# Optimization experiments

Hardware: AMD Instinct MI355X
Metric: run time of the kernel (lower is better)

## Reference

```python
import jax, jax.numpy as jnp
import numpy as np

B, S, I, H, O, L = 64, 512, 256, 512, 256, 2


def setup_inputs() -> dict:
    key = jax.random.key(0)
    ks = jax.random.split(key, 8)
    s = 0.02
    return {
        "x": jax.random.normal(ks[0], (B, S, I), dtype=jnp.float32),
        "input_W": jax.random.normal(ks[1], (H, I), dtype=jnp.float32) * s,
        "input_b": jnp.zeros((H,), dtype=jnp.float32),
        "i2h_W": jax.random.normal(ks[2], (L, H, H), dtype=jnp.float32) * s,
        "h2h_W": jax.random.normal(ks[3], (L, H, H), dtype=jnp.float32) * s,
        "h2h_b": jnp.zeros((L, H), dtype=jnp.float32),
        "out_W": jax.random.normal(ks[4], (O, H), dtype=jnp.float32) * s,
        "out_b": jnp.zeros((O,), dtype=jnp.float32),
    }


def reference(x, input_W, input_b, i2h_W, h2h_W, h2h_b, out_W, out_b):
    # input projection applied to the whole sequence at once, as in the source
    xe = jnp.einsum("bsi,hi->bsh", x, input_W) + input_b  # [B,S,H]

    def step(h, x_t):  # h: [L,B,H], x_t: [B,H]
        cur = x_t
        new_h = []
        for l in range(L):
            cur = jnp.tanh(cur @ i2h_W[l].T + h[l] @ h2h_W[l].T + h2h_b[l])
            new_h.append(cur)
        return jnp.stack(new_h), None

    h0 = jnp.zeros((L, B, H), dtype=x.dtype)
    hT, _ = jax.lax.scan(step, h0, jnp.swapaxes(xe, 0, 1))  # scan over S
    output = hT[-1] @ out_W.T + out_b  # [B,O]
    return output, hT
```

## Files before the change

### kernel.cpp

```cpp
#include <hip/hip_runtime.h>

typedef __attribute__((ext_vector_type(8))) short bf16x8;
typedef __attribute__((ext_vector_type(4))) float f32x4;

#define NWG 128

__device__ __forceinline__ unsigned short f2bf(float f) {
  union { float f; unsigned u; } v; v.f = f;
  unsigned r = v.u + 0x7FFFu + ((v.u >> 16) & 1u);
  return (unsigned short)(r >> 16);
}

__device__ __forceinline__ float bf2f(unsigned short u) {
  union { unsigned u; float f; } v; v.u = (unsigned)u << 16;
  return v.f;
}

__device__ __forceinline__ float fast_tanh(float x) {
  float ax = fminf(fabsf(x), 15.f);
  float e = __expf(2.f * ax);
  float t = (e - 1.f) / (e + 1.f);
  return copysignf(t, x);
}

#define LDH(d, b, O) \
  asm volatile("global_load_dwordx4 %0, %1, off offset:" #O " sc1" : "=v"(d) : "v"(b))
#define LDH16(A, B)            \
  LDH(A[0], B, 0);   LDH(A[1], B, 64);  LDH(A[2], B, 128); LDH(A[3], B, 192);  \
  LDH(A[4], B, 256); LDH(A[5], B, 320); LDH(A[6], B, 384); LDH(A[7], B, 448);  \
  LDH(A[8], B, 512); LDH(A[9], B, 576); LDH(A[10], B, 640); LDH(A[11], B, 704); \
  LDH(A[12], B, 768); LDH(A[13], B, 832); LDH(A[14], B, 896); LDH(A[15], B, 960)

__device__ __forceinline__ void wait_flags(const unsigned* p, unsigned tgt) {
  while (true) {
    unsigned v;
    asm volatile("global_load_dword %0, %1, off sc1\n\t"
                 "s_waitcnt vmcnt(0)"
                 : "=v"(v) : "v"(p) : "memory");
    if (__all((int)(v >= tgt))) break;
  }
}

__global__ void prep_kernel(const float* __restrict__ i2h,
                            const float* __restrict__ h2h,
                            unsigned short* __restrict__ WiB,
                            unsigned short* __restrict__ WhB,
                            unsigned short* __restrict__ h0,
                            unsigned short* __restrict__ h1,
                            unsigned* __restrict__ bar,
                            unsigned* __restrict__ flags) {
  int i = blockIdx.x * 256 + threadIdx.x;
  WiB[i] = f2bf(i2h[i]);
  WhB[i] = f2bf(h2h[i]);
  if (i < 65536) { h0[i] = 0; h1[i] = 0; }
  if (i < 64) bar[i] = 0;
  if (i < 4096) flags[i] = 0;
}

__global__ __launch_bounds__(256) void wc_kernel(const float* __restrict__ inW,
                                                 const float* __restrict__ inb,
                                                 const float* __restrict__ i2h,
                                                 const float* __restrict__ hb,
                                                 unsigned short* __restrict__ WcB,
                                                 float* __restrict__ bc) {
  const int n = blockIdx.x, i = threadIdx.x;
  const float* wrow = i2h + (size_t)n * 512;
  float acc = 0.f;
  for (int k = 0; k < 512; ++k) acc += wrow[k] * inW[k * 256 + i];
  WcB[n * 256 + i] = f2bf(acc);
  if (i == 0) {
    float a2 = 0.f;
    for (int k = 0; k < 512; ++k) a2 += wrow[k] * inb[k];
    bc[n] = a2 + hb[n];
  }
}

__global__ __launch_bounds__(256) void proj_kernel(const float* __restrict__ x,
                                                   const unsigned short* __restrict__ WcB,
                                                   const float* __restrict__ bc,
                                                   unsigned short* __restrict__ U) {
  const int tid = threadIdx.x;
  const int ln = tid & 63, wv = tid >> 6;
  const int wid = blockIdx.x * 4 + wv;
  const int mt = wid >> 5, nt = wid & 31;
  const int mrow = ln & 15, quad = ln >> 4, koff = quad * 8;
  const float* arow = x + (size_t)(mt * 16 + mrow) * 256 + koff;
  const unsigned short* brow = WcB + (size_t)(nt * 16 + mrow) * 256 + koff;
  f32x4 acc = {0.f, 0.f, 0.f, 0.f};
#pragma unroll
  for (int kk = 0; kk < 8; ++kk) {
    const int ko = kk * 32;
    bf16x8 af;
#pragma unroll
    for (int j = 0; j < 8; ++j) af[j] = (short)f2bf(arow[ko + j]);
    bf16x8 bf = *(const bf16x8*)(brow + ko);
    acc = __builtin_amdgcn_mfma_f32_16x16x32_bf16(af, bf, acc, 0, 0, 0);
  }
  const int n = nt * 16 + mrow;
  const float bias = bc[n];
  const int m0 = mt * 16 + quad * 4;
#pragma unroll
  for (int r = 0; r < 4; ++r) {
    const int m = m0 + r;
    const int b = m >> 9, s = m & 511;
    U[((size_t)(s * 64 + b) << 9) + n] = f2bf(acc[r] + bias);
  }
}

__device__ __forceinline__ void heavy_barrier(unsigned* bar) {
  __builtin_amdgcn_s_waitcnt(0);
  __syncthreads();
  if (threadIdx.x == 0) {
    __threadfence();
    unsigned prev = __hip_atomic_fetch_add(bar, 1u, __ATOMIC_RELAXED, __HIP_MEMORY_SCOPE_AGENT);
    if (prev == NWG - 1) {
      __hip_atomic_store(bar + 32, 1u, __ATOMIC_RELAXED, __HIP_MEMORY_SCOPE_AGENT);
    } else {
      while (__hip_atomic_load(bar + 32, __ATOMIC_RELAXED, __HIP_MEMORY_SCOPE_AGENT) < 1u)
        __builtin_amdgcn_s_sleep(1);
    }
    __threadfence();
  }
  __syncthreads();
}

__device__ __forceinline__ void store_h_coh(unsigned* dbase, int rowbase, int colp,
                                            bool evenl,
                                            float v0, float v1, float v2, float v3) {
  unsigned lo = (unsigned)f2bf(v0) | ((unsigned)f2bf(v1) << 16);
  unsigned hi = (unsigned)f2bf(v2) | ((unsigned)f2bf(v3) << 16);
  unsigned send = evenl ? hi : lo;
  unsigned recv = __shfl_xor(send, 1, 64);
  unsigned w0, w1; int rb;
  if (evenl) {
    w0 = (lo & 0xffffu) | (recv << 16);
    w1 = (lo >> 16) | (recv & 0xffff0000u);
    rb = rowbase;
  } else {
    w0 = (recv & 0xffffu) | (hi << 16);
    w1 = (recv >> 16) | (hi & 0xffff0000u);
    rb = rowbase + 2;
  }
  unsigned* p = dbase + rb * 256 + colp;
  __hip_atomic_store(p, w0, __ATOMIC_RELAXED, __HIP_MEMORY_SCOPE_AGENT);
  __hip_atomic_store(p + 256, w1, __ATOMIC_RELAXED, __HIP_MEMORY_SCOPE_AGENT);
}

__global__ __launch_bounds__(64, 1) void scan_kernel(const unsigned short* __restrict__ U,
                                                     const unsigned short* __restrict__ WiB,
                                                     const unsigned short* __restrict__ WhB,
                                                     const float* __restrict__ hb,
                                                     const float* __restrict__ outW,
                                                     const float* __restrict__ outb,
                                                     unsigned short* __restrict__ h0,
                                                     unsigned short* __restrict__ h1,
                                                     float* __restrict__ out,
                                                     unsigned* __restrict__ bar,
                                                     unsigned* __restrict__ flags) {
  const int ln = threadIdx.x;
  const int wid = blockIdx.x;
  const int rt = wid & 3;
  const int ct = wid >> 2;
  const int mrow = ln & 15, quad = ln >> 4, koff = quad * 8;
  const int bA = rt * 16 + mrow;
  const int n = ct * 16 + mrow;
  const bool evenl = (ln & 1) == 0;
  const int colp = n >> 1;
  const int rowbase = rt * 16 + quad * 4;

  bf16x8 wf0[16], wf1[16], wf2[16];
  {
    const unsigned short* w0 = WhB + (size_t)n * 512 + koff;
    const unsigned short* w1 = WiB + (size_t)262144 + (size_t)n * 512 + koff;
    const unsigned short* w2 = WhB + (size_t)262144 + (size_t)n * 512 + koff;
#pragma unroll
    for (int kk = 0; kk < 16; ++kk) {
      wf0[kk] = *(const bf16x8*)(w0 + kk * 32);
      wf1[kk] = *(const bf16x8*)(w1 + kk * 32);
      wf2[kk] = *(const bf16x8*)(w2 + kk * 32);
    }
  }
  const float bias1 = hb[512 + n];
  const unsigned short* h0b = h0 + (size_t)bA * 512 + koff;
  const unsigned short* h1b = h1 + (size_t)bA * 512 + koff;
  const unsigned short* UB = U + ((size_t)rowbase << 9) + n;
  unsigned* myflag = flags + ((rt * 32 + ct) << 5);
  const unsigned* pollp = flags + ((rt * 32 + (ln & 31)) << 5);

  unsigned short up0 = UB[0], up1 = UB[512], up2 = UB[1024], up3 = UB[1536];

  for (int s = 0; s <= 512; ++s) {
    const int pd = s & 1, ps = pd ^ 1;
    const bool D0 = (s < 512), D1 = (s > 0);
    if (s) wait_flags(pollp, (unsigned)s);

    const unsigned short* aH0 = h0b + (ps << 15);
    const unsigned short* aH1 = h1b + (pd << 15);
    bf16x8 h0f[16], h1f[16];
    LDH16(h0f, aH0);
    LDH16(h1f, aH1);

    asm volatile("s_waitcnt vmcnt(16)" ::: "memory");
#pragma unroll
    for (int kk = 0; kk < 16; ++kk) asm volatile("" : "+v"(h0f[kk]));

    f32x4 z = {0.f, 0.f, 0.f, 0.f};
    f32x4 acc0 = z, a1a = z, a1b = z;
#pragma unroll
    for (int kk = 0; kk < 16; ++kk) {
      if (D0) acc0 = __builtin_amdgcn_mfma_f32_16x16x32_bf16(h0f[kk], wf0[kk], acc0, 0, 0, 0);
      if (D1) a1a = __builtin_amdgcn_mfma_f32_16x16x32_bf16(h0f[kk], wf1[kk], a1a, 0, 0, 0);
    }

    if (D0) {
      float v0 = fast_tanh(acc0[0] + bf2f(up0));
      float v1 = fast_tanh(acc0[1] + bf2f(up1));
      float v2 = fast_tanh(acc0[2] + bf2f(up2));
      float v3 = fast_tanh(acc0[3] + bf2f(up3));
      store_h_coh((unsigned*)h0 + (pd << 14), rowbase, colp, evenl, v0, v1, v2, v3);
      if (s == 511) {
        float* o = out + 16384 + rowbase * 512 + n;
        o[0] = v0; o[512] = v1; o[1024] = v2; o[1536] = v3;
      }
    }

    if (D1) {
      asm volatile("s_waitcnt vmcnt(0)" ::: "memory");
#pragma unroll
      for (int kk = 0; kk < 16; ++kk) asm volatile("" : "+v"(h1f[kk]));
#pragma unroll
      for (int kk = 0; kk < 16; ++kk)
        a1b = __builtin_amdgcn_mfma_f32_16x16x32_bf16(h1f[kk], wf2[kk], a1b, 0, 0, 0);
      float v0 = fast_tanh(a1a[0] + a1b[0] + bias1);
      float v1 = fast_tanh(a1a[1] + a1b[1] + bias1);
      float v2 = fast_tanh(a1a[2] + a1b[2] + bias1);
      float v3 = fast_tanh(a1a[3] + a1b[3] + bias1);
      store_h_coh((unsigned*)h1 + (ps << 14), rowbase, colp, evenl, v0, v1, v2, v3);
      if (s == 512) {
        float* o = out + 16384 + 32768 + rowbase * 512 + n;
        o[0] = v0; o[512] = v1; o[1024] = v2; o[1536] = v3;
      }
    }

    asm volatile("s_waitcnt vmcnt(0)" ::: "memory");
    if (ln == 0) {
      unsigned fv = (unsigned)(s + 1);
      asm volatile("global_store_dword %0, %1, off sc1" :: "v"(myflag), "v"(fv) : "memory");
    }

    if (s <= 510) {
      const unsigned short* un = UB + ((size_t)(s + 1) << 15);
      up0 = un[0]; up1 = un[512]; up2 = un[1024]; up3 = un[1536];
    }
  }

  heavy_barrier(bar);

  const int g = blockIdx.x * 64 + ln;
  const float* hT1 = out + 16384 + 32768;
#pragma unroll
  for (int e = 0; e < 2; ++e) {
    const int idx = g + e * 8192;
    const int b = idx >> 8, o = idx & 255;
    const float* hr = hT1 + (b << 9);
    const float* wr = outW + (o << 9);
    float s0 = 0.f, s1 = 0.f;
    for (int k = 0; k < 512; k += 8) {
      float4 h4 = *(const float4*)(hr + k);
      float4 w4 = *(const float4*)(wr + k);
      s0 += h4.x * w4.x + h4.y * w4.y + h4.z * w4.z + h4.w * w4.w;
      float4 h5 = *(const float4*)(hr + k + 4);
      float4 w5 = *(const float4*)(wr + k + 4);
      s1 += h5.x * w5.x + h5.y * w5.y + h5.z * w5.z + h5.w * w5.w;
    }
    out[idx] = s0 + s1 + outb[o];
  }
}

extern "C" void kernel_launch(void* const* d_in, const int* in_sizes, int n_in,
                              void* d_out, int out_size, void* d_ws, size_t ws_size,
                              hipStream_t stream) {
  const float* x = (const float*)d_in[0];
  const float* inW = (const float*)d_in[1];
  const float* inb = (const float*)d_in[2];
  const float* i2h = (const float*)d_in[3];
  const float* h2h = (const float*)d_in[4];
  const float* hbias = (const float*)d_in[5];
  const float* outW = (const float*)d_in[6];
  const float* outb = (const float*)d_in[7];
  float* out = (float*)d_out;

  char* w = (char*)d_ws;
  unsigned short* WiB = (unsigned short*)w;
  unsigned short* WhB = (unsigned short*)(w + (1u << 20));
  unsigned short* WcB = (unsigned short*)(w + (2u << 20));
  float* bc = (float*)(w + (2u << 20) + (256u << 10));
  unsigned short* h0 = (unsigned short*)(w + (2u << 20) + (260u << 10));
  unsigned short* h1 = (unsigned short*)(w + (2u << 20) + (388u << 10));
  unsigned* bar = (unsigned*)(w + (2u << 20) + (516u << 10));
  unsigned* flags = (unsigned*)(w + (2u << 20) + (520u << 10));
  unsigned short* U = (unsigned short*)(w + (2u << 20) + (576u << 10));

  prep_kernel<<<2048, 256, 0, stream>>>(i2h, h2h, WiB, WhB, h0, h1, bar, flags);
  wc_kernel<<<512, 256, 0, stream>>>(inW, inb, i2h, hbias, WcB, bc);
  proj_kernel<<<16384, 256, 0, stream>>>(x, WcB, bc, U);
  scan_kernel<<<NWG, 64, 0, stream>>>(U, WiB, WhB, hbias, outW, outb, h0, h1, out, bar, flags);
}
```

Baseline: 2.109 ms.

## Split scan over 256 workgroups with XCC-local fast coherence path

Doubles the scan grid to 256 single-wave workgroups, each now owning 8 batch rows instead of 16, so per-step work is spread over more CUs. At startup it reads the XCC id of each workgroup and checks whether all groups sharing a batch tile sit on the same XCC. It then tests flag and data visibility with plain loads after buffer_inv. If that test passes, the recurrence loop uses non-sc1 stores and loads, which avoids device-scope coherence traffic. Otherwise it falls back to the sc1 path. This adds a startup handshake, bounded spin budgets that could silently break out early, and half the MFMA rows go to waste.

```diff
diff --git a/kernel.cpp b/kernel.cpp
--- a/kernel.cpp
+++ b/kernel.cpp
@@ -3,7 +3,9 @@
 typedef __attribute__((ext_vector_type(8))) short bf16x8;
 typedef __attribute__((ext_vector_type(4))) float f32x4;
 
-#define NWG 128
+#define NWG 256
+
+template <bool B> struct BoolC { static constexpr bool value = B; };
 
 __device__ __forceinline__ unsigned short f2bf(float f) {
   union { float f; unsigned u; } v; v.f = f;
@@ -23,21 +25,67 @@
   return copysignf(t, x);
 }
 
-#define LDH(d, b, O) \
+#define LDH_F(d, b, O) \
+  asm volatile("global_load_dwordx4 %0, %1, off offset:" #O : "=v"(d) : "v"(b))
+#define LDH_S(d, b, O) \
   asm volatile("global_load_dwordx4 %0, %1, off offset:" #O " sc1" : "=v"(d) : "v"(b))
-#define LDH16(A, B)            \
-  LDH(A[0], B, 0);   LDH(A[1], B, 64);  LDH(A[2], B, 128); LDH(A[3], B, 192);  \
-  LDH(A[4], B, 256); LDH(A[5], B, 320); LDH(A[6], B, 384); LDH(A[7], B, 448);  \
-  LDH(A[8], B, 512); LDH(A[9], B, 576); LDH(A[10], B, 640); LDH(A[11], B, 704); \
-  LDH(A[12], B, 768); LDH(A[13], B, 832); LDH(A[14], B, 896); LDH(A[15], B, 960)
-
-__device__ __forceinline__ void wait_flags(const unsigned* p, unsigned tgt) {
+#define LDH16_F(A, B)            \
+  LDH_F(A[0], B, 0);   LDH_F(A[1], B, 64);  LDH_F(A[2], B, 128); LDH_F(A[3], B, 192);  \
+  LDH_F(A[4], B, 256); LDH_F(A[5], B, 320); LDH_F(A[6], B, 384); LDH_F(A[7], B, 448);  \
+  LDH_F(A[8], B, 512); LDH_F(A[9], B, 576); LDH_F(A[10], B, 640); LDH_F(A[11], B, 704); \
+  LDH_F(A[12], B, 768); LDH_F(A[13], B, 832); LDH_F(A[14], B, 896); LDH_F(A[15], B, 960)
+#define LDH16_S(A, B)            \
+  LDH_S(A[0], B, 0);   LDH_S(A[1], B, 64);  LDH_S(A[2], B, 128); LDH_S(A[3], B, 192);  \
+  LDH_S(A[4], B, 256); LDH_S(A[5], B, 320); LDH_S(A[6], B, 384); LDH_S(A[7], B, 448);  \
+  LDH_S(A[8], B, 512); LDH_S(A[9], B, 576); LDH_S(A[10], B, 640); LDH_S(A[11], B, 704); \
+  LDH_S(A[12], B, 768); LDH_S(A[13], B, 832); LDH_S(A[14], B, 896); LDH_S(A[15], B, 960)
+
+template <bool FAST>
+__device__ __forceinline__ void poll_flags(const unsigned* p, unsigned tgt, int& budget) {
   while (true) {
     unsigned v;
-    asm volatile("global_load_dword %0, %1, off sc1\n\t"
-                 "s_waitcnt vmcnt(0)"
-                 : "=v"(v) : "v"(p) : "memory");
+    if (FAST)
+      asm volatile("buffer_inv sc0\n\t"
+                   "s_waitcnt vmcnt(0)\n\t"
+                   "global_load_dword %0, %1, off\n\t"
+                   "s_waitcnt vmcnt(0)" : "=v"(v) : "v"(p) : "memory");
+    else
+      asm volatile("global_load_dword %0, %1, off sc1\n\t"
+                   "s_waitcnt vmcnt(0)" : "=v"(v) : "v"(p) : "memory");
     if (__all((int)(v >= tgt))) break;
+    if (--budget < 0) break;
+  }
+}
+
+template <bool FAST>
+__device__ __forceinline__ void st2h(unsigned* p, unsigned w0, unsigned w1) {
+  if (FAST) {
+    asm volatile("global_store_dword %0, %1, off" :: "v"(p), "v"(w0) : "memory");
+    asm volatile("global_store_dword %0, %1, off offset:1024" :: "v"(p), "v"(w1) : "memory");
+  } else {
+    asm volatile("global_store_dword %0, %1, off sc1" :: "v"(p), "v"(w0) : "memory");
+    asm volatile("global_store_dword %0, %1, off offset:1024 sc1" :: "v"(p), "v"(w1) : "memory");
+  }
+}
+
+template <bool FAST>
+__device__ __forceinline__ void st_flag(unsigned* p, unsigned v) {
+  if (FAST) asm volatile("global_store_dword %0, %1, off" :: "v"(p), "v"(v) : "memory");
+  else      asm volatile("global_store_dword %0, %1, off sc1" :: "v"(p), "v"(v) : "memory");
+}
+
+__device__ __forceinline__ void packpair(bool evenl, float v0, float v1, float v2, float v3,
+                                         unsigned& w0, unsigned& w1) {
+  unsigned lo = (unsigned)f2bf(v0) | ((unsigned)f2bf(v1) << 16);
+  unsigned hi = (unsigned)f2bf(v2) | ((unsigned)f2bf(v3) << 16);
+  unsigned send = evenl ? hi : lo;
+  unsigned recv = __shfl_xor(send, 1, 64);
+  if (evenl) {
+    w0 = (lo & 0xffffu) | (recv << 16);
+    w1 = (lo >> 16) | (recv & 0xffff0000u);
+  } else {
+    w0 = (recv & 0xffffu) | (hi << 16);
+    w1 = (recv >> 16) | (hi & 0xffff0000u);
   }
 }
 
@@ -54,7 +102,7 @@
   WhB[i] = f2bf(h2h[i]);
   if (i < 65536) { h0[i] = 0; h1[i] = 0; }
   if (i < 64) bar[i] = 0;
-  if (i < 4096) flags[i] = 0;
+  if (i < 8704) flags[i] = 0;
 }
 
 __global__ __launch_bounds__(256) void wc_kernel(const float* __restrict__ inW,
@@ -107,43 +155,24 @@
   }
 }
 
-__device__ __forceinline__ void heavy_barrier(unsigned* bar) {
+__device__ __forceinline__ void heavy_barrier(unsigned* bar, int slot) {
   __builtin_amdgcn_s_waitcnt(0);
   __syncthreads();
   if (threadIdx.x == 0) {
     __threadfence();
-    unsigned prev = __hip_atomic_fetch_add(bar, 1u, __ATOMIC_RELAXED, __HIP_MEMORY_SCOPE_AGENT);
+    unsigned prev = __hip_atomic_fetch_add(bar + slot, 1u, __ATOMIC_RELAXED, __HIP_MEMORY_SCOPE_AGENT);
     if (prev == NWG - 1) {
-      __hip_atomic_store(bar + 32, 1u, __ATOMIC_RELAXED, __HIP_MEMORY_SCOPE_AGENT);
+      __hip_atomic_store(bar + 16 + slot, 1u, __ATOMIC_RELAXED, __HIP_MEMORY_SCOPE_AGENT);
     } else {
-      while (__hip_atomic_load(bar + 32, __ATOMIC_RELAXED, __HIP_MEMORY_SCOPE_AGENT) < 1u)
+      int b = 1 << 22;
+      while (__hip_atomic_load(bar + 16 + slot, __ATOMIC_RELAXED, __HIP_MEMORY_SCOPE_AGENT) < 1u) {
         __builtin_amdgcn_s_sleep(1);
+        if (--b < 0) break;
+      }
     }
     __threadfence();
   }
   __syncthreads();
-}
-
-__device__ __forceinline__ void store_h_coh(unsigned* dbase, int rowbase, int colp,
-                                            bool evenl,
-                                            float v0, float v1, float v2, float v3) {
-  unsigned lo = (unsigned)f2bf(v0) | ((unsigned)f2bf(v1) << 16);
-  unsigned hi = (unsigned)f2bf(v2) | ((unsigned)f2bf(v3) << 16);
-  unsigned send = evenl ? hi : lo;
-  unsigned recv = __shfl_xor(send, 1, 64);
-  unsigned w0, w1; int rb;
-  if (evenl) {
-    w0 = (lo & 0xffffu) | (recv << 16);
-    w1 = (lo >> 16) | (recv & 0xffff0000u);
-    rb = rowbase;
-  } else {
-    w0 = (recv & 0xffffu) | (hi << 16);
-    w1 = (recv >> 16) | (hi & 0xffff0000u);
-    rb = rowbase + 2;
-  }
-  unsigned* p = dbase + rb * 256 + colp;
-  __hip_atomic_store(p, w0, __ATOMIC_RELAXED, __HIP_MEMORY_SCOPE_AGENT);
-  __hip_atomic_store(p + 256, w1, __ATOMIC_RELAXED, __HIP_MEMORY_SCOPE_AGENT);
 }
 
 __global__ __launch_bounds__(64, 1) void scan_kernel(const unsigned short* __restrict__ U,
@@ -159,14 +188,15 @@
                                                      unsigned* __restrict__ flags) {
   const int ln = threadIdx.x;
   const int wid = blockIdx.x;
-  const int rt = wid & 3;
-  const int ct = wid >> 2;
+  const int rt = wid & 7;
+  const int ct = wid >> 3;
   const int mrow = ln & 15, quad = ln >> 4, koff = quad * 8;
-  const int bA = rt * 16 + mrow;
+  const int bA = rt * 8 + (mrow & 7);
   const int n = ct * 16 + mrow;
   const bool evenl = (ln & 1) == 0;
   const int colp = n >> 1;
-  const int rowbase = rt * 16 + quad * 4;
+  const int hrow = quad * 4;
+  const int urow = rt * 8 + ((quad & 1) << 2);
 
   bf16x8 wf0[16], wf1[16], wf2[16];
   {
@@ -183,98 +213,157 @@
   const float bias1 = hb[512 + n];
   const unsigned short* h0b = h0 + (size_t)bA * 512 + koff;
   const unsigned short* h1b = h1 + (size_t)bA * 512 + koff;
-  const unsigned short* UB = U + ((size_t)rowbase << 9) + n;
-  unsigned* myflag = flags + ((rt * 32 + ct) << 5);
-  const unsigned* pollp = flags + ((rt * 32 + (ln & 31)) << 5);
+  const unsigned short* UB = U + ((size_t)urow << 9) + n;
+  unsigned* myflag = flags + ((rt * 32 + ct) << 4);
+  const unsigned* pollp = flags + ((rt * 32 + (ln & 31)) << 4);
+  unsigned* mydata = flags + 4096 + ((rt * 32 + ct) << 4);
+  const unsigned* datap = flags + 4096 + ((rt * 32 + (ln & 31)) << 4);
+  unsigned* xbuf = flags + 8192;
+  unsigned* xbuf2 = flags + 8448;
+
+  unsigned xcc = __builtin_amdgcn_s_getreg(6164) & 0xFu;
+  if (ln == 0)
+    __hip_atomic_store(xbuf + wid, xcc | 16u, __ATOMIC_RELAXED, __HIP_MEMORY_SCOPE_AGENT);
+  heavy_barrier(bar, 0);
+  unsigned xv = __hip_atomic_load(xbuf + ((ln & 31) * 8 + rt), __ATOMIC_RELAXED, __HIP_MEMORY_SCOPE_AGENT);
+  unsigned xp = __hip_atomic_load(xbuf + (wid ^ 1), __ATOMIC_RELAXED, __HIP_MEMORY_SCOPE_AGENT);
+  unsigned x0 = __shfl(xv, 0, 64);
+  const bool cand = __all((int)(xv == x0)) && (xp != (xcc | 16u));
+
+  bool ok = cand;
+  if (cand) {
+    int pb = 1 << 13;
+    for (int r = 1; r <= 3 && ok; ++r) {
+      unsigned pat = 0xA5A50000u + (unsigned)r;
+      if (ln == 0) {
+        asm volatile("global_store_dword %0, %1, off" :: "v"(mydata), "v"(pat) : "memory");
+        asm volatile("s_waitcnt vmcnt(0)" ::: "memory");
+        asm volatile("global_store_dword %0, %1, off" :: "v"(myflag), "v"((unsigned)r) : "memory");
+      }
+      bool got = false;
+      while (true) {
+        unsigned v;
+        asm volatile("buffer_inv sc0\n\ts_waitcnt vmcnt(0)\n\t"
+                     "global_load_dword %0, %1, off\n\ts_waitcnt vmcnt(0)"
+                     : "=v"(v) : "v"(pollp) : "memory");
+        if (__all((int)(v >= (unsigned)r))) { got = true; break; }
+        if (--pb < 0) break;
+      }
+      if (!got) { ok = false; break; }
+      unsigned d;
+      asm volatile("global_load_dword %0, %1, off\n\ts_waitcnt vmcnt(0)"
+                   : "=v"(d) : "v"(datap) : "memory");
+      if (!__all((int)(d == pat))) ok = false;
+    }
+  }
+
+  if (ln == 0)
+    __hip_atomic_store(xbuf2 + wid, ok ? 2u : 1u, __ATOMIC_RELAXED, __HIP_MEMORY_SCOPE_AGENT);
+  heavy_barrier(bar, 2);
+  unsigned av = __hip_atomic_load(xbuf2 + ((ln & 31) * 8 + rt), __ATOMIC_RELAXED, __HIP_MEMORY_SCOPE_AGENT);
+  const bool fastpath = __all((int)(av == 2u));
 
   unsigned short up0 = UB[0], up1 = UB[512], up2 = UB[1024], up3 = UB[1536];
-
-  for (int s = 0; s <= 512; ++s) {
-    const int pd = s & 1, ps = pd ^ 1;
-    const bool D0 = (s < 512), D1 = (s > 0);
-    if (s) wait_flags(pollp, (unsigned)s);
-
-    const unsigned short* aH0 = h0b + (ps << 15);
-    const unsigned short* aH1 = h1b + (pd << 15);
-    bf16x8 h0f[16], h1f[16];
-    LDH16(h0f, aH0);
-    LDH16(h1f, aH1);
-
-    asm volatile("s_waitcnt vmcnt(16)" ::: "memory");
-#pragma unroll
-    for (int kk = 0; kk < 16; ++kk) asm volatile("" : "+v"(h0f[kk]));
-
-    f32x4 z = {0.f, 0.f, 0.f, 0.f};
-    f32x4 acc0 = z, a1a = z, a1b = z;
-#pragma unroll
-    for (int kk = 0; kk < 16; ++kk) {
-      if (D0) acc0 = __builtin_amdgcn_mfma_f32_16x16x32_bf16(h0f[kk], wf0[kk], acc0, 0, 0, 0);
-      if (D1) a1a = __builtin_amdgcn_mfma_f32_16x16x32_bf16(h0f[kk], wf1[kk], a1a, 0, 0, 0);
+  float t00 = 0, t01 = 0, t02 = 0, t03 = 0, t10 = 0, t11 = 0, t12 = 0, t13 = 0;
+  int pbudget = 1 << 19;
+
+  auto loop = [&](auto FC) {
+    constexpr bool FAST = decltype(FC)::value;
+    for (int s = 0; s <= 512; ++s) {
+      const int pd = s & 1, ps = pd ^ 1;
+      const bool D0 = (s < 512), D1 = (s > 0);
+      if (s) poll_flags<FAST>(pollp, (unsigned)(s + 3), pbudget);
+      else if (FAST) asm volatile("buffer_inv sc0\n\ts_waitcnt vmcnt(0)" ::: "memory");
+      asm volatile("" : "+v"(up0), "+v"(up1), "+v"(up2), "+v"(up3));
+
+      bf16x8 h0f[16], h1f[16];
+      const unsigned short* aH0 = h0b + (ps << 15);
+      const unsigned short* aH1 = h1b + (pd << 15);
+      if (FAST) { LDH16_F(h0f, aH0); LDH16_F(h1f, aH1); }
+      else      { LDH16_S(h0f, aH0); LDH16_S(h1f, aH1); }
+
+      asm volatile("s_waitcnt vmcnt(16)" ::: "memory");
+#pragma unroll
+      for (int kk = 0; kk < 16; ++kk) asm volatile("" : "+v"(h0f[kk]));
+
+      f32x4 z = {0.f, 0.f, 0.f, 0.f};
+      f32x4 acc0 = z, a1a = z, a1b = z;
+#pragma unroll
+      for (int kk = 0; kk < 16; ++kk) {
+        if (D0) acc0 = __builtin_amdgcn_mfma_f32_16x16x32_bf16(h0f[kk], wf0[kk], acc0, 0, 0, 0);
+        if (D1) a1a = __builtin_amdgcn_mfma_f32_16x16x32_bf16(h0f[kk], wf1[kk], a1a, 0, 0, 0);
+      }
+
+      if (D0) {
+        float v0 = fast_tanh(acc0[0] + bf2f(up0));
+        float v1 = fast_tanh(acc0[1] + bf2f(up1));
+        float v2 = fast_tanh(acc0[2] + bf2f(up2));
+        float v3 = fast_tanh(acc0[3] + bf2f(up3));
+        unsigned w0, w1;
+        packpair(evenl, v0, v1, v2, v3, w0, w1);
+        if (quad < 2) {
+          int row = rt * 8 + hrow + (evenl ? 0 : 2);
+          st2h<FAST>((unsigned*)h0 + (pd << 14) + row * 256 + colp, w0, w1);
+        }
+        if (s == 511) { t00 = v0; t01 = v1; t02 = v2; t03 = v3; }
+      }
+
+      if (D0) asm volatile("s_waitcnt vmcnt(2)" ::: "memory");
+      else    asm volatile("s_waitcnt vmcnt(0)" ::: "memory");
+#pragma unroll
+      for (int kk = 0; kk < 16; ++kk) asm volatile("" : "+v"(h1f[kk]));
+
+      if (D1) {
+#pragma unroll
+        for (int kk = 0; kk < 16; ++kk)
+          a1b = __builtin_amdgcn_mfma_f32_16x16x32_bf16(h1f[kk], wf2[kk], a1b, 0, 0, 0);
+        float v0 = fast_tanh(a1a[0] + a1b[0] + bias1);
+        float v1 = fast_tanh(a1a[1] + a1b[1] + bias1);
+        float v2 = fast_tanh(a1a[2] + a1b[2] + bias1);
+        float v3 = fast_tanh(a1a[3] + a1b[3] + bias1);
+        unsigned w0, w1;
+        packpair(evenl, v0, v1, v2, v3, w0, w1);
+        if (quad < 2) {
+          int row = rt * 8 + hrow + (evenl ? 0 : 2);
+          st2h<FAST>((unsigned*)h1 + (ps << 14) + row * 256 + colp, w0, w1);
+        }
+        if (s == 512) { t10 = v0; t11 = v1; t12 = v2; t13 = v3; }
+      }
+
+      asm volatile("s_waitcnt vmcnt(0)" ::: "memory");
+      if (ln == 0) st_flag<FAST>(myflag, (unsigned)(s + 4));
+
+      if (s <= 510) {
+        const unsigned short* un = UB + ((size_t)(s + 1) << 15);
+        up0 = un[0]; up1 = un[512]; up2 = un[1024]; up3 = un[1536];
+      }
     }
-
-    if (D0) {
-      float v0 = fast_tanh(acc0[0] + bf2f(up0));
-      float v1 = fast_tanh(acc0[1] + bf2f(up1));
-      float v2 = fast_tanh(acc0[2] + bf2f(up2));
-      float v3 = fast_tanh(acc0[3] + bf2f(up3));
-      store_h_coh((unsigned*)h0 + (pd << 14), rowbase, colp, evenl, v0, v1, v2, v3);
-      if (s == 511) {
-        float* o = out + 16384 + rowbase * 512 + n;
-        o[0] = v0; o[512] = v1; o[1024] = v2; o[1536] = v3;
-      }
-    }
-
-    if (D1) {
-      asm volatile("s_waitcnt vmcnt(0)" ::: "memory");
-#pragma unroll
-      for (int kk = 0; kk < 16; ++kk) asm volatile("" : "+v"(h1f[kk]));
-#pragma unroll
-      for (int kk = 0; kk < 16; ++kk)
-        a1b = __builtin_amdgcn_mfma_f32_16x16x32_bf16(h1f[kk], wf2[kk], a1b, 0, 0, 0);
-      float v0 = fast_tanh(a1a[0] + a1b[0] + bias1);
-      float v1 = fast_tanh(a1a[1] + a1b[1] + bias1);
-      float v2 = fast_tanh(a1a[2] + a1b[2] + bias1);
-      float v3 = fast_tanh(a1a[3] + a1b[3] + bias1);
-      store_h_coh((unsigned*)h1 + (ps << 14), rowbase, colp, evenl, v0, v1, v2, v3);
-      if (s == 512) {
-        float* o = out + 16384 + 32768 + rowbase * 512 + n;
-        o[0] = v0; o[512] = v1; o[1024] = v2; o[1536] = v3;
-      }
-    }
-
-    asm volatile("s_waitcnt vmcnt(0)" ::: "memory");
-    if (ln == 0) {
-      unsigned fv = (unsigned)(s + 1);
-      asm volatile("global_store_dword %0, %1, off sc1" :: "v"(myflag), "v"(fv) : "memory");
-    }
-
-    if (s <= 510) {
-      const unsigned short* un = UB + ((size_t)(s + 1) << 15);
-      up0 = un[0]; up1 = un[512]; up2 = un[1024]; up3 = un[1536];
-    }
-  }
-
-  heavy_barrier(bar);
-
-  const int g = blockIdx.x * 64 + ln;
-  const float* hT1 = out + 16384 + 32768;
-#pragma unroll
-  for (int e = 0; e < 2; ++e) {
-    const int idx = g + e * 8192;
-    const int b = idx >> 8, o = idx & 255;
-    const float* hr = hT1 + (b << 9);
-    const float* wr = outW + (o << 9);
-    float s0 = 0.f, s1 = 0.f;
-    for (int k = 0; k < 512; k += 8) {
-      float4 h4 = *(const float4*)(hr + k);
-      float4 w4 = *(const float4*)(wr + k);
-      s0 += h4.x * w4.x + h4.y * w4.y + h4.z * w4.z + h4.w * w4.w;
-      float4 h5 = *(const float4*)(hr + k + 4);
-      float4 w5 = *(const float4*)(wr + k + 4);
-      s1 += h5.x * w5.x + h5.y * w5.y + h5.z * w5.z + h5.w * w5.w;
-    }
-    out[idx] = s0 + s1 + outb[o];
-  }
+  };
+  if (fastpath) loop(BoolC<true>{});
+  else          loop(BoolC<false>{});
+
+  if (quad < 2) {
+    float* o = out + 16384 + (size_t)(rt * 8 + hrow) * 512 + n;
+    o[0] = t00; o[512] = t01; o[1024] = t02; o[1536] = t03;
+    float* o1 = o + 32768;
+    o1[0] = t10; o1[512] = t11; o1[1024] = t12; o1[1536] = t13;
+  }
+  heavy_barrier(bar, 1);
+
+  const int idx = wid * 64 + ln;
+  const int b = idx >> 8, o = idx & 255;
+  const float* hr = out + 16384 + 32768 + (b << 9);
+  const float* wr = outW + (o << 9);
+  float s0 = 0.f, s1 = 0.f;
+  for (int k = 0; k < 512; k += 8) {
+    float4 h4 = *(const float4*)(hr + k);
+    float4 w4 = *(const float4*)(wr + k);
+    s0 += h4.x * w4.x + h4.y * w4.y + h4.z * w4.z + h4.w * w4.w;
+    float4 h5 = *(const float4*)(hr + k + 4);
+    float4 w5 = *(const float4*)(wr + k + 4);
+    s1 += h5.x * w5.x + h5.y * w5.y + h5.z * w5.z + h5.w * w5.w;
+  }
+  out[idx] = s0 + s1 + outb[o];
 }
 
 extern "C" void kernel_launch(void* const* d_in, const int* in_sizes, int n_in,
```

After: 3.117 ms. 47.8% more time.
